# Kernel optimization log

Measured on AMD Instinct MI355X. Metric: run time of the kernel, lower is better.

Reference implementation:

```python
import jax, jax.numpy as jnp
import numpy as np

NX, NY = 4096, 4096
DX, DY, DT = 1e-3, 1e-3, 5e-4


def setup_inputs() -> dict:
    key = jax.random.key(0)
    k1, k2, k3, k4 = jax.random.split(key, 4)
    shp = (1, 1, NX, NY)
    return {
        "Ez": jax.random.normal(k1, shp, dtype=jnp.float32),
        "Hx": jax.random.normal(k2, shp, dtype=jnp.float32),
        "Hy": jax.random.normal(k3, shp, dtype=jnp.float32),
        "eps": jnp.ones(shp, dtype=jnp.float32),
        "mu": jnp.ones(shp, dtype=jnp.float32),
        "sigma": jax.random.uniform(k4, shp, dtype=jnp.float32),
    }


def _ddx(f, inv2dx):
    # central difference along axis 0, zero on all boundary cells
    # (matches the sparse stencil which is only populated for interior rows)
    d = jnp.zeros_like(f)
    return d.at[1:-1, 1:-1].set((f[2:, 1:-1] - f[:-2, 1:-1]) * inv2dx)


def _ddy(f, inv2dy):
    d = jnp.zeros_like(f)
    return d.at[1:-1, 1:-1].set((f[1:-1, 2:] - f[1:-1, :-2]) * inv2dy)


def reference(Ez, Hx, Hy, eps, mu, sigma):
    ez = Ez[0, 0]
    hx = Hx[0, 0]
    hy = Hy[0, 0]
    eps2 = eps[0, 0]
    mu2 = mu[0, 0]
    sig2 = sigma[0, 0]
    inv2dx = 1.0 / (2.0 * DX)
    inv2dy = 1.0 / (2.0 * DY)

    # H updates from curl of Ez
    hx_new = hx - DT * (_ddy(ez, inv2dy) / mu2)
    hy_new = hy + DT * (_ddx(ez, inv2dx) / mu2)

    # Ez update from curl of H (lossy medium semi-implicit coefficients)
    curl_z = _ddx(hy_new, inv2dx) - _ddy(hx_new, inv2dy)
    A_plus = 1.0 + sig2 * DT / (2.0 * eps2)
    A_minus = 1.0 - sig2 * DT / (2.0 * eps2)
    ez_new = (A_minus / A_plus) * ez + (DT / (A_plus * eps2)) * curl_z

    shp = (1, 1, NX, NY)
    return (ez_new.reshape(shp), hx_new.reshape(shp), hy_new.reshape(shp))
```

## Files before the change

### kernel.cpp

```cpp
#include <hip/hip_runtime.h>

#define NXg 4096
#define NYg 4096

__global__ __launch_bounds__(256) void fdtd_step_kernel(
    const float* __restrict__ ez, const float* __restrict__ hx,
    const float* __restrict__ hy, const float* __restrict__ eps,
    const float* __restrict__ mu, const float* __restrict__ sigma,
    float* __restrict__ ez_out, float* __restrict__ hx_out,
    float* __restrict__ hy_out)
{
    const int j = blockIdx.x * blockDim.x + threadIdx.x;
    const int i = blockIdx.y;
    if (j >= NYg) return;
    const long idx = (long)i * NYg + j;

    constexpr float DT = 5e-4f;
    constexpr float DX = 1e-3f;
    constexpr float DY = 1e-3f;
    const float inv2dx = 1.0f / (2.0f * DX);
    const float inv2dy = 1.0f / (2.0f * DY);

    const bool jin = (j >= 1) && (j < NYg - 1);
    const bool iin = (i >= 1) && (i < NXg - 1);
    const bool interior = iin && jin;

    const float ezC = ez[idx];
    const float invmuC = 1.0f / mu[idx];

    const float ddy_ezC = interior ? (ez[idx + 1] - ez[idx - 1]) * inv2dy : 0.0f;
    const float ddx_ezC = interior ? (ez[idx + NYg] - ez[idx - NYg]) * inv2dx : 0.0f;

    const float hx_new = hx[idx] - DT * ddy_ezC * invmuC;
    const float hy_new = hy[idx] + DT * ddx_ezC * invmuC;

    float curl = 0.0f;
    if (interior) {
        const float dExP = (i < NXg - 2) ? (ez[idx + 2 * NYg] - ezC) * inv2dx : 0.0f;
        const float dExM = (i >= 2)      ? (ezC - ez[idx - 2 * NYg]) * inv2dx : 0.0f;
        const float hyP = hy[idx + NYg] + DT * dExP / mu[idx + NYg];
        const float hyM = hy[idx - NYg] + DT * dExM / mu[idx - NYg];

        const float dEyP = (j < NYg - 2) ? (ez[idx + 2] - ezC) * inv2dy : 0.0f;
        const float dEyM = (j >= 2)      ? (ezC - ez[idx - 2]) * inv2dy : 0.0f;
        const float hxP = hx[idx + 1] - DT * dEyP / mu[idx + 1];
        const float hxM = hx[idx - 1] - DT * dEyM / mu[idx - 1];

        curl = (hyP - hyM) * inv2dx - (hxP - hxM) * inv2dy;
    }

    const float ep = eps[idx];
    const float s  = sigma[idx] * DT / (2.0f * ep);
    const float Ap = 1.0f + s;
    const float Am = 1.0f - s;
    const float ez_new = (Am / Ap) * ezC + (DT / (Ap * ep)) * curl;

    ez_out[idx] = ez_new;
    hx_out[idx] = hx_new;
    hy_out[idx] = hy_new;
}

extern "C" void kernel_launch(void* const* d_in, const int* in_sizes, int n_in,
                              void* d_out, int out_size, void* d_ws, size_t ws_size,
                              hipStream_t stream) {
    const float* ez    = (const float*)d_in[0];
    const float* hx    = (const float*)d_in[1];
    const float* hy    = (const float*)d_in[2];
    const float* eps   = (const float*)d_in[3];
    const float* mu    = (const float*)d_in[4];
    const float* sigma = (const float*)d_in[5];

    const long N = (long)NXg * NYg;
    float* out    = (float*)d_out;
    float* ez_out = out;
    float* hx_out = out + N;
    float* hy_out = out + 2 * N;

    dim3 block(256, 1, 1);
    dim3 grid(NYg / 256, NXg, 1);
    fdtd_step_kernel<<<grid, block, 0, stream>>>(ez, hx, hy, eps, mu, sigma,
                                                 ez_out, hx_out, hy_out);
}
```

Before: 515.7 us.

## Vectorize FDTD stencil to float4 per thread with nontemporal stores and fast reciprocals

Each thread now processes four consecutive columns, loading neighbor rows and left/right float4 chunks of ez, hx and mu. The stencil values are then extracted from small register windows. Divisions are replaced with hardware reciprocal approximations, and outputs are written with nontemporal vector stores. The aim is fewer, wider memory transactions for this bandwidth-bound kernel. In exchange it issues extra neighbor vector loads, and the approximate reciprocals may change results slightly.

```diff
diff --git a/kernel.cpp b/kernel.cpp
--- a/kernel.cpp
+++ b/kernel.cpp
@@ -2,6 +2,8 @@
 
 #define NXg 4096
 #define NYg 4096
+
+typedef float v4f __attribute__((ext_vector_type(4)));
 
 __global__ __launch_bounds__(256) void fdtd_step_kernel(
     const float* __restrict__ ez, const float* __restrict__ hx,
@@ -10,54 +12,104 @@
     float* __restrict__ ez_out, float* __restrict__ hx_out,
     float* __restrict__ hy_out)
 {
-    const int j = blockIdx.x * blockDim.x + threadIdx.x;
-    const int i = blockIdx.y;
-    if (j >= NYg) return;
-    const long idx = (long)i * NYg + j;
+    const int j0 = (blockIdx.x * blockDim.x + threadIdx.x) * 4;
+    const int i  = blockIdx.y;
+    const long row = (long)i * NYg;
+    const long idx = row + j0;
 
     constexpr float DT = 5e-4f;
-    constexpr float DX = 1e-3f;
-    constexpr float DY = 1e-3f;
-    const float inv2dx = 1.0f / (2.0f * DX);
-    const float inv2dy = 1.0f / (2.0f * DY);
+    constexpr float inv2dx = 500.0f;
+    constexpr float inv2dy = 500.0f;
 
-    const bool jin = (j >= 1) && (j < NYg - 1);
     const bool iin = (i >= 1) && (i < NXg - 1);
-    const bool interior = iin && jin;
+    const bool iP2 = (i < NXg - 2);
+    const bool iM2 = (i >= 2);
 
-    const float ezC = ez[idx];
-    const float invmuC = 1.0f / mu[idx];
+    const int rm1 = (i >= 1) ? i - 1 : i;
+    const int rp1 = (i < NXg - 1) ? i + 1 : i;
+    const int rm2 = (i >= 2) ? i - 2 : i;
+    const int rp2 = (i < NXg - 2) ? i + 2 : i;
 
-    const float ddy_ezC = interior ? (ez[idx + 1] - ez[idx - 1]) * inv2dy : 0.0f;
-    const float ddx_ezC = interior ? (ez[idx + NYg] - ez[idx - NYg]) * inv2dx : 0.0f;
+    const long jm = (j0 == 0) ? (long)j0 : (long)j0 - 4;
+    const long jp = (j0 == NYg - 4) ? (long)j0 : (long)j0 + 4;
 
-    const float hx_new = hx[idx] - DT * ddy_ezC * invmuC;
-    const float hy_new = hy[idx] + DT * ddx_ezC * invmuC;
+    const v4f ezL  = *(const v4f*)(ez + row + jm);
+    const v4f ezC4 = *(const v4f*)(ez + idx);
+    const v4f ezR  = *(const v4f*)(ez + row + jp);
+    const v4f ezU  = *(const v4f*)(ez + (long)rp1 * NYg + j0);
+    const v4f ezD  = *(const v4f*)(ez + (long)rm1 * NYg + j0);
+    const v4f ezU2 = *(const v4f*)(ez + (long)rp2 * NYg + j0);
+    const v4f ezD2 = *(const v4f*)(ez + (long)rm2 * NYg + j0);
 
-    float curl = 0.0f;
-    if (interior) {
-        const float dExP = (i < NXg - 2) ? (ez[idx + 2 * NYg] - ezC) * inv2dx : 0.0f;
-        const float dExM = (i >= 2)      ? (ezC - ez[idx - 2 * NYg]) * inv2dx : 0.0f;
-        const float hyP = hy[idx + NYg] + DT * dExP / mu[idx + NYg];
-        const float hyM = hy[idx - NYg] + DT * dExM / mu[idx - NYg];
+    const v4f hxL  = *(const v4f*)(hx + row + jm);
+    const v4f hxC4 = *(const v4f*)(hx + idx);
+    const v4f hxR  = *(const v4f*)(hx + row + jp);
 
-        const float dEyP = (j < NYg - 2) ? (ez[idx + 2] - ezC) * inv2dy : 0.0f;
-        const float dEyM = (j >= 2)      ? (ezC - ez[idx - 2]) * inv2dy : 0.0f;
-        const float hxP = hx[idx + 1] - DT * dEyP / mu[idx + 1];
-        const float hxM = hx[idx - 1] - DT * dEyM / mu[idx - 1];
+    const v4f hyC4 = *(const v4f*)(hy + idx);
+    const v4f hyU  = *(const v4f*)(hy + (long)rp1 * NYg + j0);
+    const v4f hyD  = *(const v4f*)(hy + (long)rm1 * NYg + j0);
 
-        curl = (hyP - hyM) * inv2dx - (hxP - hxM) * inv2dy;
+    const v4f muL  = *(const v4f*)(mu + row + jm);
+    const v4f muC4 = *(const v4f*)(mu + idx);
+    const v4f muR  = *(const v4f*)(mu + row + jp);
+    const v4f muU  = *(const v4f*)(mu + (long)rp1 * NYg + j0);
+    const v4f muD  = *(const v4f*)(mu + (long)rm1 * NYg + j0);
+
+    const v4f ep4  = *(const v4f*)(eps + idx);
+    const v4f sg4  = *(const v4f*)(sigma + idx);
+
+    float ezw[12], hxw[12], muw[12];
+    *(v4f*)&ezw[0] = ezL;  *(v4f*)&ezw[4] = ezC4;  *(v4f*)&ezw[8] = ezR;
+    *(v4f*)&hxw[0] = hxL;  *(v4f*)&hxw[4] = hxC4;  *(v4f*)&hxw[8] = hxR;
+    *(v4f*)&muw[0] = muL;  *(v4f*)&muw[4] = muC4;  *(v4f*)&muw[8] = muR;
+
+    v4f ezo, hxo, hyo;
+
+#pragma unroll
+    for (int e = 0; e < 4; ++e) {
+        const int j = j0 + e;
+        const bool jin = (j >= 1) && (j < NYg - 1);
+        const bool interior = iin && jin;
+
+        const float ezCv  = ezw[e + 4];
+        const float invmu = __builtin_amdgcn_rcpf(muw[e + 4]);
+
+        const float ddy = interior ? (ezw[e + 5] - ezw[e + 3]) * inv2dy : 0.0f;
+        const float ddx = interior ? (ezU[e] - ezD[e]) * inv2dx : 0.0f;
+
+        const float hx_new = hxw[e + 4] - DT * ddy * invmu;
+        const float hy_new = hyC4[e]    + DT * ddx * invmu;
+
+        float curl = 0.0f;
+        if (interior) {
+            const float dExP = iP2 ? (ezU2[e] - ezCv) * inv2dx : 0.0f;
+            const float dExM = iM2 ? (ezCv - ezD2[e]) * inv2dx : 0.0f;
+            const float hyP = hyU[e] + DT * dExP * __builtin_amdgcn_rcpf(muU[e]);
+            const float hyM = hyD[e] + DT * dExM * __builtin_amdgcn_rcpf(muD[e]);
+
+            const float dEyP = (j < NYg - 2) ? (ezw[e + 6] - ezCv) * inv2dy : 0.0f;
+            const float dEyM = (j >= 2)      ? (ezCv - ezw[e + 2]) * inv2dy : 0.0f;
+            const float hxP = hxw[e + 5] - DT * dEyP * __builtin_amdgcn_rcpf(muw[e + 5]);
+            const float hxM = hxw[e + 3] - DT * dEyM * __builtin_amdgcn_rcpf(muw[e + 3]);
+
+            curl = (hyP - hyM) * inv2dx - (hxP - hxM) * inv2dy;
+        }
+
+        const float ep  = ep4[e];
+        const float rep = __builtin_amdgcn_rcpf(ep);
+        const float s   = sg4[e] * DT * 0.5f * rep;
+        const float Ap  = 1.0f + s;
+        const float Am  = 1.0f - s;
+        const float rAp = __builtin_amdgcn_rcpf(Ap);
+
+        ezo[e] = Am * rAp * ezCv + DT * rAp * rep * curl;
+        hxo[e] = hx_new;
+        hyo[e] = hy_new;
     }
 
-    const float ep = eps[idx];
-    const float s  = sigma[idx] * DT / (2.0f * ep);
-    const float Ap = 1.0f + s;
-    const float Am = 1.0f - s;
-    const float ez_new = (Am / Ap) * ezC + (DT / (Ap * ep)) * curl;
-
-    ez_out[idx] = ez_new;
-    hx_out[idx] = hx_new;
-    hy_out[idx] = hy_new;
+    __builtin_nontemporal_store(ezo, (v4f*)(ez_out + idx));
+    __builtin_nontemporal_store(hxo, (v4f*)(hx_out + idx));
+    __builtin_nontemporal_store(hyo, (v4f*)(hy_out + idx));
 }
 
 extern "C" void kernel_launch(void* const* d_in, const int* in_sizes, int n_in,
@@ -77,7 +129,7 @@
     float* hy_out = out + 2 * N;
 
     dim3 block(256, 1, 1);
-    dim3 grid(NYg / 256, NXg, 1);
+    dim3 grid(NYg / (256 * 4), NXg, 1);
     fdtd_step_kernel<<<grid, block, 0, stream>>>(ez, hx, hy, eps, mu, sigma,
                                                  ez_out, hx_out, hy_out);
 }
```

New measurement: 460.5 us. -10.7%, faster.
